# Kernel tuning notes

Measured on AMD Instinct MI355X. Metric: run time of the kernel, lower is better.

## Reference

```python
import jax, jax.numpy as jnp
import numpy as np

PICK_WIN = 20      # int(round(pick_win_s / dt)) = int(round(2.0 / 0.1))
W_PICK = 0.1
BETA = 25.0


def setup_inputs() -> dict:
    key = jax.random.key(0)
    k1, k2 = jax.random.split(key)
    B, T = 4096, 6000
    pred = jax.random.normal(k1, (B, T), dtype=jnp.float32)
    target = jax.random.normal(k2, (B, T), dtype=jnp.float32)
    return {"pred": pred, "target": target}


def _windowed_soft_argmax(x, mask, pos):
    # soft_argmax(|x[s:e]|, beta) + s  ==  sum_j softmax(beta*|x_j| over j in [s,e)) * j
    logits = jnp.where(mask, BETA * jnp.abs(x), -jnp.inf)  # [B, T]
    p = jax.nn.softmax(logits, axis=-1)
    return jnp.sum(p * pos.astype(x.dtype), axis=-1)       # [B]


def reference(pred, target):
    loss = jnp.mean(jnp.abs(pred - target))  # nn.L1Loss (mean)

    T = target.shape[-1]
    center = jnp.argmax(jnp.abs(target), axis=-1)          # [B]
    pos = jnp.arange(T)                                     # [T]
    # window [max(0, c-W), min(T, c+W)) expressed as a mask over absolute positions
    mask = (pos[None, :] >= center[:, None] - PICK_WIN) & (pos[None, :] < center[:, None] + PICK_WIN)

    picks_pred = _windowed_soft_argmax(pred, mask, pos)
    picks_true = _windowed_soft_argmax(target, mask, pos)

    pick_loss = jnp.mean(jnp.abs(picks_pred - picks_true)) / T
    return loss + W_PICK * pick_loss
```

## Files before the change

### kernel.cpp

```cpp
#include <hip/hip_runtime.h>
#include <math.h>
#include <limits.h>
#include <stdint.h>

#define T_LEN 6000
#define B_ROWS 4096
#define PICK_WIN 20
#define BETA 25.0f

typedef float f4 __attribute__((ext_vector_type(4)));

__global__ __launch_bounds__(128) void row_pass1(const float* __restrict__ pred,
                                                 const float* __restrict__ target,
                                                 float* __restrict__ row_l1,
                                                 float* __restrict__ row_pick) {
    const int row  = blockIdx.x;
    const int tid  = threadIdx.x;
    const int wave = tid >> 6;
    const int lane = tid & 63;

    const uint64_t pb = (uint64_t)(pred   + (size_t)row * T_LEN);
    const uint64_t tb = (uint64_t)(target + (size_t)row * T_LEN);

    const bool has12 = (tid < (T_LEN / 4 - 11 * 128));
    uint32_t va[12];
    #pragma unroll
    for (int k = 0; k < 11; ++k) va[k] = (uint32_t)(tid + k * 128) * 16u;
    va[11] = has12 ? (uint32_t)(tid + 11 * 128) * 16u
                   : (uint32_t)((T_LEN / 4 - 1) * 16);

    f4 p0, p1, p2, p3, p4, p5, p6, p7, p8, p9, p10, p11;
    f4 t0, t1, t2, t3, t4, t5, t6, t7, t8, t9, t10, t11;

    asm volatile(
        "global_load_dwordx4 %0,  %12, %18\n\t"
        "global_load_dwordx4 %6,  %12, %19\n\t"
        "global_load_dwordx4 %1,  %13, %18\n\t"
        "global_load_dwordx4 %7,  %13, %19\n\t"
        "global_load_dwordx4 %2,  %14, %18\n\t"
        "global_load_dwordx4 %8,  %14, %19\n\t"
        "global_load_dwordx4 %3,  %15, %18\n\t"
        "global_load_dwordx4 %9,  %15, %19\n\t"
        "global_load_dwordx4 %4,  %16, %18\n\t"
        "global_load_dwordx4 %10, %16, %19\n\t"
        "global_load_dwordx4 %5,  %17, %18\n\t"
        "global_load_dwordx4 %11, %17, %19"
        : "=&v"(p0), "=&v"(p1), "=&v"(p2), "=&v"(p3), "=&v"(p4), "=&v"(p5),
          "=&v"(t0), "=&v"(t1), "=&v"(t2), "=&v"(t3), "=&v"(t4), "=&v"(t5)
        : "v"(va[0]), "v"(va[1]), "v"(va[2]), "v"(va[3]), "v"(va[4]), "v"(va[5]),
          "s"(pb), "s"(tb));
    asm volatile(
        "global_load_dwordx4 %0,  %12, %18\n\t"
        "global_load_dwordx4 %6,  %12, %19\n\t"
        "global_load_dwordx4 %1,  %13, %18\n\t"
        "global_load_dwordx4 %7,  %13, %19\n\t"
        "global_load_dwordx4 %2,  %14, %18\n\t"
        "global_load_dwordx4 %8,  %14, %19\n\t"
        "global_load_dwordx4 %3,  %15, %18\n\t"
        "global_load_dwordx4 %9,  %15, %19\n\t"
        "global_load_dwordx4 %4,  %16, %18\n\t"
        "global_load_dwordx4 %10, %16, %19\n\t"
        "global_load_dwordx4 %5,  %17, %18\n\t"
        "global_load_dwordx4 %11, %17, %19"
        : "=&v"(p6), "=&v"(p7), "=&v"(p8), "=&v"(p9), "=&v"(p10), "=&v"(p11),
          "=&v"(t6), "=&v"(t7), "=&v"(t8), "=&v"(t9), "=&v"(t10), "=&v"(t11)
        : "v"(va[6]), "v"(va[7]), "v"(va[8]), "v"(va[9]), "v"(va[10]), "v"(va[11]),
          "s"(pb), "s"(tb));

    float sum   = 0.0f;
    float bestv = -1.0f;
    int   besti = INT_MAX;

#define CONSUME(PP, TT, K)                                                     \
    do {                                                                       \
        const int base = (tid + (K) * 128) * 4;                                \
        sum += fabsf(PP.x - TT.x) + fabsf(PP.y - TT.y) +                       \
               fabsf(PP.z - TT.z) + fabsf(PP.w - TT.w);                        \
        float a_;                                                              \
        a_ = fabsf(TT.x); if (a_ > bestv) { bestv = a_; besti = base;     }    \
        a_ = fabsf(TT.y); if (a_ > bestv) { bestv = a_; besti = base + 1; }    \
        a_ = fabsf(TT.z); if (a_ > bestv) { bestv = a_; besti = base + 2; }    \
        a_ = fabsf(TT.w); if (a_ > bestv) { bestv = a_; besti = base + 3; }    \
    } while (0)

    asm volatile("s_waitcnt vmcnt(12)" ::: "memory");
    __builtin_amdgcn_sched_barrier(0);
    CONSUME(p0, t0, 0);
    CONSUME(p1, t1, 1);
    CONSUME(p2, t2, 2);
    CONSUME(p3, t3, 3);
    CONSUME(p4, t4, 4);
    CONSUME(p5, t5, 5);

    asm volatile("s_waitcnt vmcnt(0)" ::: "memory");
    __builtin_amdgcn_sched_barrier(0);
    CONSUME(p6,  t6,  6);
    CONSUME(p7,  t7,  7);
    CONSUME(p8,  t8,  8);
    CONSUME(p9,  t9,  9);
    CONSUME(p10, t10, 10);
    if (has12) CONSUME(p11, t11, 11);
#undef CONSUME

    #pragma unroll
    for (int o = 32; o > 0; o >>= 1) {
        sum += __shfl_xor(sum, o);
        const float ov = __shfl_xor(bestv, o);
        const int   oi = __shfl_xor(besti, o);
        if (ov > bestv || (ov == bestv && oi < besti)) { bestv = ov; besti = oi; }
    }

    __shared__ float s_sum[2];
    __shared__ float s_val[2];
    __shared__ int   s_idx[2];
    if (lane == 0) { s_sum[wave] = sum; s_val[wave] = bestv; s_idx[wave] = besti; }
    __syncthreads();

    if (tid < 64) {
        float bs = s_sum[0] + s_sum[1];
        float bv = s_val[0];
        int   bi = s_idx[0];
        if (s_val[1] > bv || (s_val[1] == bv && s_idx[1] < bi)) {
            bv = s_val[1]; bi = s_idx[1];
        }

        const int c   = bi;
        const int s   = max(0, c - PICK_WIN);
        const int e   = min(T_LEN, c + PICK_WIN);
        const int len = e - s;

        float ap = -INFINITY, at = -INFINITY;
        const float posf = (float)(s + tid);
        if (tid < len) {
            const size_t idx = (size_t)row * T_LEN + s + tid;
            ap = BETA * fabsf(pred[idx]);
            at = BETA * fabsf(target[idx]);
        }

        float mp = ap, mt = at;
        #pragma unroll
        for (int o = 32; o > 0; o >>= 1) {
            mp = fmaxf(mp, __shfl_xor(mp, o));
            mt = fmaxf(mt, __shfl_xor(mt, o));
        }

        float wp = 0.0f, wt = 0.0f, wpp = 0.0f, wtp = 0.0f;
        if (tid < len) {
            wp  = expf(ap - mp);
            wt  = expf(at - mt);
            wpp = wp * posf;
            wtp = wt * posf;
        }
        #pragma unroll
        for (int o = 32; o > 0; o >>= 1) {
            wp  += __shfl_xor(wp,  o);
            wt  += __shfl_xor(wt,  o);
            wpp += __shfl_xor(wpp, o);
            wtp += __shfl_xor(wtp, o);
        }

        if (tid == 0) {
            row_l1[row]   = bs;
            row_pick[row] = fabsf(wpp / wp - wtp / wt);
        }
    }
}

__global__ __launch_bounds__(256) void finalize(const float* __restrict__ row_l1,
                                                const float* __restrict__ row_pick,
                                                float* __restrict__ out) {
    const int tid  = threadIdx.x;
    const int wave = tid >> 6;
    const int lane = tid & 63;
    const f4* l4 = (const f4*)row_l1;
    const f4* p4 = (const f4*)row_pick;

    float a = 0.0f, b = 0.0f;
    #pragma unroll
    for (int k = 0; k < 4; ++k) {
        const f4 x = l4[tid + k * 256];
        const f4 y = p4[tid + k * 256];
        a += x.x + x.y + x.z + x.w;
        b += y.x + y.y + y.z + y.w;
    }
    #pragma unroll
    for (int o = 32; o > 0; o >>= 1) {
        a += __shfl_xor(a, o);
        b += __shfl_xor(b, o);
    }
    __shared__ float f1[4], f2[4];
    if (lane == 0) { f1[wave] = a; f2[wave] = b; }
    __syncthreads();
    if (tid == 0) {
        const float ta = f1[0] + f1[1] + f1[2] + f1[3];
        const float tb = f2[0] + f2[1] + f2[2] + f2[3];
        const float loss = ta / (float)((long long)B_ROWS * (long long)T_LEN);
        const float pick = (tb / (float)B_ROWS) / (float)T_LEN;
        out[0] = loss + 0.1f * pick;
    }
}

extern "C" void kernel_launch(void* const* d_in, const int* in_sizes, int n_in,
                              void* d_out, int out_size, void* d_ws, size_t ws_size,
                              hipStream_t stream) {
    const float* pred   = (const float*)d_in[0];
    const float* target = (const float*)d_in[1];
    float* out = (float*)d_out;

    float* row_l1   = (float*)d_ws;
    float* row_pick = row_l1 + B_ROWS;

    row_pass1<<<B_ROWS, 128, 0, stream>>>(pred, target, row_l1, row_pick);
    finalize<<<1, 256, 0, stream>>>(row_l1, row_pick, out);
}
```

Measured before the change: 37.84 us.

## Fuse final reduction into row kernel via fixed-point atomics and last-block detection

Result: slower. 43.28 us (+14.4%).

```diff
diff --git a/kernel.cpp b/kernel.cpp
--- a/kernel.cpp
+++ b/kernel.cpp
@@ -7,13 +7,16 @@
 #define B_ROWS 4096
 #define PICK_WIN 20
 #define BETA 25.0f
+#define SCALE_L1 2097152.0f
+#define SCALE_PK 67108864.0f
+#define GRP_STRIDE 256
 
 typedef float f4 __attribute__((ext_vector_type(4)));
 
-__global__ __launch_bounds__(128) void row_pass1(const float* __restrict__ pred,
-                                                 const float* __restrict__ target,
-                                                 float* __restrict__ row_l1,
-                                                 float* __restrict__ row_pick) {
+__global__ __launch_bounds__(128) void fused_loss(const float* __restrict__ pred,
+                                                  const float* __restrict__ target,
+                                                  char* __restrict__ cnts,
+                                                  float* __restrict__ out) {
     const int row  = blockIdx.x;
     const int tid  = threadIdx.x;
     const int wave = tid >> 6;
@@ -160,43 +163,47 @@
         }
 
         if (tid == 0) {
-            row_l1[row]   = bs;
-            row_pick[row] = fabsf(wpp / wp - wtp / wt);
-        }
-    }
-}
-
-__global__ __launch_bounds__(256) void finalize(const float* __restrict__ row_l1,
-                                                const float* __restrict__ row_pick,
-                                                float* __restrict__ out) {
-    const int tid  = threadIdx.x;
-    const int wave = tid >> 6;
-    const int lane = tid & 63;
-    const f4* l4 = (const f4*)row_l1;
-    const f4* p4 = (const f4*)row_pick;
-
-    float a = 0.0f, b = 0.0f;
-    #pragma unroll
-    for (int k = 0; k < 4; ++k) {
-        const f4 x = l4[tid + k * 256];
-        const f4 y = p4[tid + k * 256];
-        a += x.x + x.y + x.z + x.w;
-        b += y.x + y.y + y.z + y.w;
-    }
-    #pragma unroll
-    for (int o = 32; o > 0; o >>= 1) {
-        a += __shfl_xor(a, o);
-        b += __shfl_xor(b, o);
-    }
-    __shared__ float f1[4], f2[4];
-    if (lane == 0) { f1[wave] = a; f2[wave] = b; }
-    __syncthreads();
-    if (tid == 0) {
-        const float ta = f1[0] + f1[1] + f1[2] + f1[3];
-        const float tb = f2[0] + f2[1] + f2[2] + f2[3];
-        const float loss = ta / (float)((long long)B_ROWS * (long long)T_LEN);
-        const float pick = (tb / (float)B_ROWS) / (float)T_LEN;
-        out[0] = loss + 0.1f * pick;
+            const float pickv = fabsf(wpp / wp - wtp / wt);
+            const unsigned long long i1 =
+                (unsigned long long)llrintf(bs * SCALE_L1);
+            const unsigned long long i2 =
+                (unsigned long long)llrintf(pickv * SCALE_PK);
+
+            unsigned long long* gl1 =
+                (unsigned long long*)(cnts + (size_t)(row >> 6) * GRP_STRIDE);
+            unsigned long long* gpk  = gl1 + 1;
+            unsigned*           gcnt = (unsigned*)(gl1 + 2);
+
+            unsigned long long r1 = atomicAdd(gl1, i1);
+            unsigned long long r2 = atomicAdd(gpk, i2);
+            asm volatile("" :: "v"(r1), "v"(r2) : "memory");
+
+            const unsigned old = atomicAdd(gcnt, 1u);
+            if (old == 63u) {
+                const unsigned long long g1 = atomicAdd(gl1, 0ull);
+                const unsigned long long g2 = atomicAdd(gpk, 0ull);
+
+                unsigned long long* tl1 =
+                    (unsigned long long*)(cnts + (size_t)64 * GRP_STRIDE);
+                unsigned long long* tpk  = tl1 + 1;
+                unsigned*           tcnt = (unsigned*)(tl1 + 2);
+
+                unsigned long long q1 = atomicAdd(tl1, g1);
+                unsigned long long q2 = atomicAdd(tpk, g2);
+                asm volatile("" :: "v"(q1), "v"(q2) : "memory");
+
+                const unsigned told = atomicAdd(tcnt, 1u);
+                if (told == 63u) {
+                    const unsigned long long s1 = atomicAdd(tl1, 0ull);
+                    const unsigned long long s2 = atomicAdd(tpk, 0ull);
+                    const double loss = ((double)s1 / (double)SCALE_L1) /
+                                        ((double)B_ROWS * (double)T_LEN);
+                    const double pick = (((double)s2 / (double)SCALE_PK) /
+                                         (double)B_ROWS) / (double)T_LEN;
+                    out[0] = (float)(loss + 0.1 * pick);
+                }
+            }
+        }
     }
 }
 
@@ -207,9 +214,8 @@
     const float* target = (const float*)d_in[1];
     float* out = (float*)d_out;
 
-    float* row_l1   = (float*)d_ws;
-    float* row_pick = row_l1 + B_ROWS;
-
-    row_pass1<<<B_ROWS, 128, 0, stream>>>(pred, target, row_l1, row_pick);
-    finalize<<<1, 256, 0, stream>>>(row_l1, row_pick, out);
+    char* cnts = (char*)d_ws;
+    hipMemsetAsync(cnts, 0, 65 * GRP_STRIDE, stream);
+
+    fused_loss<<<B_ROWS, 128, 0, stream>>>(pred, target, cnts, out);
 }
```
